# Performance work log

Measured on AMD Instinct MI355X. Metric: run time of the kernel, lower is better.

Reference implementation:

```python
import jax, jax.numpy as jnp
import numpy as np

E = 600000
N = 50000
H = 128
OE = 256


def swish(v):
    return v * jax.nn.sigmoid(v)


def setup_inputs() -> dict:
    key = jax.random.key(0)
    ks = jax.random.split(key, 16)
    inp = {
        "x": jax.random.normal(ks[0], (E, H), dtype=jnp.float32),
        "rbf": jax.random.normal(ks[1], (E, 6), dtype=jnp.float32),
        "i": jax.random.randint(ks[2], (E,), 0, N, dtype=jnp.int32),
        "edge_index": jax.random.randint(ks[3], (2, E), 0, N, dtype=jnp.int32),
        "edge_weight": jax.random.uniform(ks[4], (E,), dtype=jnp.float32),
        "batch": jax.random.randint(ks[5], (N,), 0, 32, dtype=jnp.int32),
        "num_nodes": N,
        "W_rbf": jax.random.normal(ks[6], (H, 6), dtype=jnp.float32) * 0.2,
        "W_up": jax.random.normal(ks[7], (OE, H), dtype=jnp.float32) * (1.0 / np.sqrt(H)),
        "b_up": jnp.zeros((OE,), dtype=jnp.float32),
        "W_l1": jax.random.normal(ks[8], (OE, OE), dtype=jnp.float32) * (1.0 / np.sqrt(OE)),
        "b_l1": jnp.zeros((OE,), dtype=jnp.float32),
        "W_l2": jax.random.normal(ks[9], (OE, OE), dtype=jnp.float32) * (1.0 / np.sqrt(OE)),
        "b_l2": jnp.zeros((OE,), dtype=jnp.float32),
        "W_l3": jax.random.normal(ks[10], (OE, OE), dtype=jnp.float32) * (1.0 / np.sqrt(OE)),
        "b_l3": jnp.zeros((OE,), dtype=jnp.float32),
        "W_out": jax.random.normal(ks[11], (1, OE), dtype=jnp.float32) * (1.0 / np.sqrt(OE)),
        "W_w": jax.random.normal(ks[12], (1, H), dtype=jnp.float32) * (1.0 / np.sqrt(H)),
        "b_w": jnp.zeros((1,), dtype=jnp.float32),
    }
    return inp


def reference(x, rbf, i, edge_index, edge_weight, batch, num_nodes,
              W_rbf, W_up, b_up, W_l1, b_l1, W_l2, b_l2, W_l3, b_l3,
              W_out, W_w, b_w):
    # edge_index / edge_weight are unused in the original forward.
    # x = lin_rbf(rbf) * x  -> [E, H]
    xe = (rbf @ W_rbf.T) * x
    # scatter-add edges -> nodes: [N, H]
    xn = jax.ops.segment_sum(xe, i, num_segments=num_nodes)
    # energy head: alpha = w_lin(x) before lin_up
    alpha = xn @ W_w.T + b_w  # [N, 1]
    x2 = xn @ W_up.T + b_up   # [N, OE]
    for W, b in ((W_l1, b_l1), (W_l2, b_l2), (W_l3, b_l3)):
        x2 = swish(x2 @ W.T + b)
    out = (x2 @ W_out.T) * alpha  # [N, 1]
    return (out, batch)
```

## Files before the change

### kernel.cpp

```cpp
#include <hip/hip_runtime.h>
#include <hip/hip_bf16.h>
#include <math.h>

#define E_CNT 600000
#define N_CNT 50000
#define H_DIM 128
#define OE_DIM 256

typedef __attribute__((ext_vector_type(8))) short short8;
typedef __attribute__((ext_vector_type(4))) float f32x4;

#define WS_OFF    0
#define WS_CNT    200016
#define WS_TEXC   400016
#define WS_BSUM   600720
#define WS_WUP    601744
#define WS_WL1    667280
#define WS_WL2    798352
#define WS_WL3    929424
#define WS_RANK   1060496
#define WS_XE     3460496

#define SCAN_NB 196
#define WCONV_NB 896

__global__ __launch_bounds__(256) void histwconv_kernel(
    const int* __restrict__ nid, int* __restrict__ counts,
    int* __restrict__ rank,
    const float* __restrict__ Wup, const float* __restrict__ Wl1,
    const float* __restrict__ Wl2, const float* __restrict__ Wl3,
    ushort* __restrict__ dUp, ushort* __restrict__ dL1,
    ushort* __restrict__ dL2, ushort* __restrict__ dL3)
{
    if (blockIdx.x < WCONV_NB) {
        int d = blockIdx.x * 256 + threadIdx.x;
        const float* W;
        ushort* dst;
        int K;
        if (d < 32768)       { W = Wup; dst = dUp; K = 128; }
        else if (d < 98304)  { d -= 32768;  W = Wl1; dst = dL1; K = 256; }
        else if (d < 163840) { d -= 98304;  W = Wl2; dst = dL2; K = 256; }
        else                 { d -= 163840; W = Wl3; dst = dL3; K = 256; }
        int j = d & 7;
        int l = (d >> 3) & 63;
        int KS = K >> 5;
        int ks = (d >> 9) % KS;
        int ot = (d >> 9) / KS;
        int k = ks * 32 + ((l >> 4) << 3) + j;
        int o = ot * 16 + (l & 15);
        __hip_bfloat16 h = __float2bfloat16(W[o * K + k]);
        dst[d] = *(const ushort*)&h;
    } else {
        int nb = gridDim.x - WCONV_NB;
        for (int e = (blockIdx.x - WCONV_NB) * 256 + threadIdx.x; e < E_CNT;
             e += nb * 256)
            rank[e] = atomicAdd(&counts[nid[e]], 1);
    }
}

__global__ __launch_bounds__(256) void scanA_kernel(const int* __restrict__ counts,
                                                    int* __restrict__ texc,
                                                    int* __restrict__ bsum)
{
    __shared__ int s[256];
    const int t = threadIdx.x;
    const int i = blockIdx.x * 256 + t;
    int v = (i < N_CNT) ? counts[i] : 0;
    s[t] = v;
    __syncthreads();
    for (int off = 1; off < 256; off <<= 1) {
        int u = (t >= off) ? s[t - off] : 0;
        __syncthreads();
        s[t] += u;
        __syncthreads();
    }
    texc[i] = s[t] - v;
    if (t == 255) bsum[blockIdx.x] = s[255];
}

__global__ __launch_bounds__(256) void scanC_kernel(const int* __restrict__ texc,
                                                    const int* __restrict__ bsum,
                                                    int* __restrict__ offs)
{
    __shared__ int red[256];
    const int t = threadIdx.x;
    int v = (t < (int)blockIdx.x && t < SCAN_NB) ? bsum[t] : 0;
    red[t] = v;
    __syncthreads();
    for (int off = 128; off >= 1; off >>= 1) {
        if (t < off) red[t] += red[t + off];
        __syncthreads();
    }
    const int boff = red[0];
    const int i = blockIdx.x * 256 + t;
    if (i < N_CNT) offs[i] = texc[i] + boff;
    if (i == 0) offs[N_CNT] = E_CNT;
}

__global__ __launch_bounds__(256, 4) void prepass_kernel(
    const float* __restrict__ x, const float* __restrict__ rbf,
    const int* __restrict__ nid, const int* __restrict__ rank,
    const int* __restrict__ offs, const float* __restrict__ W_rbf,
    ushort* __restrict__ xep)
{
    const int tid = threadIdx.x;
    const int lane = tid & 63;
    const int q = lane >> 4;
    const int p = lane & 15;
    const int h0 = p * 8;

    float wrb[8][6];
#pragma unroll
    for (int j = 0; j < 8; ++j)
#pragma unroll
        for (int k = 0; k < 6; ++k)
            wrb[j][k] = W_rbf[(h0 + j) * 6 + k];

    const int wid = (blockIdx.x * 256 + tid) >> 6;
    const int nw = (gridDim.x * 256) >> 6;
    const int nquad = E_CNT / 4;

    for (int t = wid; t < nquad; t += nw) {
        const int e = t * 4 + q;
        const int slot = offs[nid[e]] + rank[e];

        const float4 xa = *(const float4*)(x + (size_t)e * H_DIM + h0);
        const float4 xb = *(const float4*)(x + (size_t)e * H_DIM + h0 + 4);
        const float2* rp = (const float2*)(rbf + (size_t)e * 6);
        const float2 q0 = rp[0], q1 = rp[1], q2 = rp[2];
        const float r[6] = {q0.x, q0.y, q1.x, q1.y, q2.x, q2.y};

        float c[8];
#pragma unroll
        for (int j = 0; j < 8; ++j) {
            float cc = 0.f;
#pragma unroll
            for (int k = 0; k < 6; ++k) cc = fmaf(r[k], wrb[j][k], cc);
            c[j] = cc;
        }
        const float xv[8] = {xa.x, xa.y, xa.z, xa.w, xb.x, xb.y, xb.z, xb.w};
        ushort pk[8];
#pragma unroll
        for (int j = 0; j < 8; ++j) {
            __hip_bfloat16 h = __float2bfloat16(c[j] * xv[j]);
            pk[j] = *(const ushort*)&h;
        }
        *(int4*)(xep + (size_t)slot * H_DIM + h0) = *(const int4*)pk;
    }
}

#define MB 32
#define PITCH 264

template<int KS, bool SW>
__device__ __forceinline__ void layer(const ushort* __restrict__ Wsh,
                                      const float* __restrict__ bias,
                                      const ushort* in_s, ushort* out_s, int tid)
{
    const int w = tid >> 6, lane = tid & 63;
    const int l15 = lane & 15, lg = lane >> 4;

    f32x4 acc[2][2];
#pragma unroll
    for (int mi = 0; mi < 2; ++mi)
#pragma unroll
        for (int oi = 0; oi < 2; ++oi)
            acc[mi][oi] = (f32x4){0.f, 0.f, 0.f, 0.f};

#pragma unroll
    for (int ks = 0; ks < KS; ++ks) {
        short8 b0 = *(const short8*)(Wsh + (size_t)(((w * 2 + 0) * KS + ks) * 64 + lane) * 8);
        short8 b1 = *(const short8*)(Wsh + (size_t)(((w * 2 + 1) * KS + ks) * 64 + lane) * 8);
#pragma unroll
        for (int mi = 0; mi < 2; ++mi) {
            short8 a = *(const short8*)(in_s + (mi * 16 + l15) * PITCH + ks * 32 + lg * 8);
            acc[mi][0] = __builtin_amdgcn_mfma_f32_16x16x32_bf16(a, b0, acc[mi][0], 0, 0, 0);
            acc[mi][1] = __builtin_amdgcn_mfma_f32_16x16x32_bf16(a, b1, acc[mi][1], 0, 0, 0);
        }
    }

#pragma unroll
    for (int oi = 0; oi < 2; ++oi) {
        float bv = bias[(w * 2 + oi) * 16 + l15];
#pragma unroll
        for (int mi = 0; mi < 2; ++mi)
#pragma unroll
            for (int r = 0; r < 4; ++r) {
                float v = acc[mi][oi][r] + bv;
                if (SW) v = v / (1.f + __expf(-v));
                __hip_bfloat16 h = __float2bfloat16(v);
                out_s[(mi * 16 + lg * 4 + r) * PITCH + (w * 2 + oi) * 16 + l15] =
                    *(const ushort*)&h;
            }
    }
}

__global__ __launch_bounds__(512, 6) void fused_kernel(
    const ushort* __restrict__ xep,
    const int* __restrict__ offs,
    const float* __restrict__ W_w, const float* __restrict__ b_w,
    const ushort* __restrict__ Wup, const ushort* __restrict__ Wl1,
    const ushort* __restrict__ Wl2, const ushort* __restrict__ Wl3,
    const float* __restrict__ b_up, const float* __restrict__ b_l1,
    const float* __restrict__ b_l2, const float* __restrict__ b_l3,
    const float* __restrict__ W_out, const int* __restrict__ batch,
    float* __restrict__ out)
{
    __shared__ ushort sA[MB * PITCH];
    __shared__ ushort sB[MB * PITCH];
    __shared__ int s_off[MB + 1];
    __shared__ float s_alpha[MB];

    const int tid = threadIdx.x;
    const int w = tid >> 6, lane = tid & 63;
    const int node0 = blockIdx.x * MB;

    if (tid < MB) {
        int node = node0 + tid;
        if (node < N_CNT) out[N_CNT + node] = (float)batch[node];
    }
    if (tid < MB + 1)
        s_off[tid] = offs[min(node0 + tid, N_CNT)];
    __syncthreads();

    {
        const int eq = lane >> 4;
        const int p = lane & 15;
        float ww[8];
#pragma unroll
        for (int j = 0; j < 8; ++j) ww[j] = W_w[p * 8 + j];
        const float bw = b_w[0];

        for (int nl4 = 0; nl4 < 4; ++nl4) {
            const int nl = (w << 2) + nl4;
            const int ls = s_off[nl], le = s_off[nl + 1];
            float acc[8];
#pragma unroll
            for (int j = 0; j < 8; ++j) acc[j] = 0.f;

#pragma unroll 2
            for (int s = ls + eq; s < le; s += 4) {
                short8 rv = *(const short8*)(xep + (size_t)s * H_DIM + p * 8);
#pragma unroll
                for (int j = 0; j < 8; ++j) {
                    ushort u = (ushort)rv[j];
                    acc[j] += __bfloat162float(*(const __hip_bfloat16*)&u);
                }
            }
#pragma unroll
            for (int j = 0; j < 8; ++j) {
                acc[j] += __shfl_xor(acc[j], 16);
                acc[j] += __shfl_xor(acc[j], 32);
            }
            float part = 0.f;
#pragma unroll
            for (int j = 0; j < 8; ++j) part = fmaf(acc[j], ww[j], part);
            part += __shfl_xor(part, 1);
            part += __shfl_xor(part, 2);
            part += __shfl_xor(part, 4);
            part += __shfl_xor(part, 8);
            if (lane == 0) s_alpha[nl] = part + bw;
            if (eq == 0) {
                ushort pk[8];
#pragma unroll
                for (int j = 0; j < 8; ++j) {
                    __hip_bfloat16 h = __float2bfloat16(acc[j]);
                    pk[j] = *(const ushort*)&h;
                }
                *(int4*)(sA + nl * PITCH + p * 8) = *(const int4*)pk;
            }
        }
    }
    __syncthreads();

    layer<4, false>(Wup, b_up, sA, sB, tid);
    __syncthreads();
    layer<8, true>(Wl1, b_l1, sB, sA, tid);
    __syncthreads();
    layer<8, true>(Wl2, b_l2, sA, sB, tid);
    __syncthreads();
    layer<8, true>(Wl3, b_l3, sB, sA, tid);
    __syncthreads();

    {
        int nl = tid >> 4, q = tid & 15;
        const ushort* rowp = sA + nl * PITCH + q * 16;
        float sum = 0.f;
#pragma unroll
        for (int o = 0; o < 16; ++o) {
            __hip_bfloat16 h = *(const __hip_bfloat16*)(rowp + o);
            sum = fmaf(__bfloat162float(h), W_out[q * 16 + o], sum);
        }
        sum += __shfl_xor(sum, 1);
        sum += __shfl_xor(sum, 2);
        sum += __shfl_xor(sum, 4);
        sum += __shfl_xor(sum, 8);
        int node = node0 + nl;
        if (q == 0 && node < N_CNT) out[node] = sum * s_alpha[nl];
    }
}

extern "C" void kernel_launch(void* const* d_in, const int* in_sizes, int n_in,
                              void* d_out, int out_size, void* d_ws, size_t ws_size,
                              hipStream_t stream)
{
    const float* x      = (const float*)d_in[0];
    const float* rbf    = (const float*)d_in[1];
    const int*   nid    = (const int*)d_in[2];
    const int*   batch  = (const int*)d_in[5];
    const float* W_rbf  = (const float*)d_in[7];
    const float* W_up   = (const float*)d_in[8];
    const float* b_up   = (const float*)d_in[9];
    const float* W_l1   = (const float*)d_in[10];
    const float* b_l1   = (const float*)d_in[11];
    const float* W_l2   = (const float*)d_in[12];
    const float* b_l2   = (const float*)d_in[13];
    const float* W_l3   = (const float*)d_in[14];
    const float* b_l3   = (const float*)d_in[15];
    const float* W_out  = (const float*)d_in[16];
    const float* W_w    = (const float*)d_in[17];
    const float* b_w    = (const float*)d_in[18];

    char* ws = (char*)d_ws;
    int*    offs   = (int*)(ws + WS_OFF);
    int*    counts = (int*)(ws + WS_CNT);
    int*    texc   = (int*)(ws + WS_TEXC);
    int*    bsum   = (int*)(ws + WS_BSUM);
    ushort* WupS   = (ushort*)(ws + WS_WUP);
    ushort* Wl1S   = (ushort*)(ws + WS_WL1);
    ushort* Wl2S   = (ushort*)(ws + WS_WL2);
    ushort* Wl3S   = (ushort*)(ws + WS_WL3);
    int*    rank   = (int*)(ws + WS_RANK);
    ushort* xep    = (ushort*)(ws + WS_XE);
    float*  out    = (float*)d_out;

    hipMemsetAsync(counts, 0, N_CNT * sizeof(int), stream);
    histwconv_kernel<<<WCONV_NB + 1024, 256, 0, stream>>>(
        nid, counts, rank, W_up, W_l1, W_l2, W_l3, WupS, Wl1S, Wl2S, Wl3S);
    scanA_kernel<<<SCAN_NB, 256, 0, stream>>>(counts, texc, bsum);
    scanC_kernel<<<SCAN_NB, 256, 0, stream>>>(texc, bsum, offs);

    prepass_kernel<<<2048, 256, 0, stream>>>(x, rbf, nid, rank, offs, W_rbf, xep);

    fused_kernel<<<(N_CNT + MB - 1) / MB, 512, 0, stream>>>(
        xep, offs, W_w, b_w,
        WupS, Wl1S, Wl2S, Wl3S, b_up, b_l1, b_l2, b_l3, W_out, batch, out);
}
```

Measured before the change: 233.9 us.

## Write edge features in original order and gather via sorted edge-id list

The prepass now writes bf16 edge features contiguously in edge order instead of scattering each row to its sorted slot, and records a sorted-slot to edge-id map. The fused kernel stages chunks of edge ids in shared memory and gathers each edge row indirectly when reducing per node. This replaces scattered 256-byte writes with coalesced writes at the cost of scattered reads, an extra int array, chunked accumulation through bf16 shared memory (possible extra rounding), and lower occupancy bounds.

```diff
diff --git a/kernel.cpp b/kernel.cpp
--- a/kernel.cpp
+++ b/kernel.cpp
@@ -19,7 +19,8 @@
 #define WS_WL2    798352
 #define WS_WL3    929424
 #define WS_RANK   1060496
-#define WS_XE     3460496
+#define WS_EIDS   3460496
+#define WS_XE     5860496
 
 #define SCAN_NB 196
 #define WCONV_NB 896
@@ -101,7 +102,7 @@
     const float* __restrict__ x, const float* __restrict__ rbf,
     const int* __restrict__ nid, const int* __restrict__ rank,
     const int* __restrict__ offs, const float* __restrict__ W_rbf,
-    ushort* __restrict__ xep)
+    ushort* __restrict__ xe16, int* __restrict__ eids)
 {
     const int tid = threadIdx.x;
     const int lane = tid & 63;
@@ -122,7 +123,9 @@
 
     for (int t = wid; t < nquad; t += nw) {
         const int e = t * 4 + q;
-        const int slot = offs[nid[e]] + rank[e];
+
+        if (p == 0)
+            eids[offs[nid[e]] + rank[e]] = e;
 
         const float4 xa = *(const float4*)(x + (size_t)e * H_DIM + h0);
         const float4 xb = *(const float4*)(x + (size_t)e * H_DIM + h0 + 4);
@@ -145,12 +148,13 @@
             __hip_bfloat16 h = __float2bfloat16(c[j] * xv[j]);
             pk[j] = *(const ushort*)&h;
         }
-        *(int4*)(xep + (size_t)slot * H_DIM + h0) = *(const int4*)pk;
+        *(int4*)(xe16 + (size_t)e * H_DIM + h0) = *(const int4*)pk;
     }
 }
 
 #define MB 32
 #define PITCH 264
+#define EMAX 640
 
 template<int KS, bool SW>
 __device__ __forceinline__ void layer(const ushort* __restrict__ Wsh,
@@ -195,9 +199,9 @@
     }
 }
 
-__global__ __launch_bounds__(512, 6) void fused_kernel(
-    const ushort* __restrict__ xep,
-    const int* __restrict__ offs,
+__global__ __launch_bounds__(512, 4) void fused_kernel(
+    const ushort* __restrict__ xe16,
+    const int* __restrict__ offs, const int* __restrict__ eids,
     const float* __restrict__ W_w, const float* __restrict__ b_w,
     const ushort* __restrict__ Wup, const ushort* __restrict__ Wl1,
     const ushort* __restrict__ Wl2, const ushort* __restrict__ Wl3,
@@ -208,6 +212,7 @@
 {
     __shared__ ushort sA[MB * PITCH];
     __shared__ ushort sB[MB * PITCH];
+    __shared__ int s_eids[EMAX];
     __shared__ int s_off[MB + 1];
     __shared__ float s_alpha[MB];
 
@@ -222,6 +227,10 @@
     if (tid < MB + 1)
         s_off[tid] = offs[min(node0 + tid, N_CNT)];
     __syncthreads();
+
+    const int s0 = s_off[0];
+    const int tot = s_off[MB] - s0;
+    const int nchunks = (tot + EMAX - 1) / EMAX;
 
     {
         const int eq = lane >> 4;
@@ -231,43 +240,67 @@
         for (int j = 0; j < 8; ++j) ww[j] = W_w[p * 8 + j];
         const float bw = b_w[0];
 
-        for (int nl4 = 0; nl4 < 4; ++nl4) {
-            const int nl = (w << 2) + nl4;
-            const int ls = s_off[nl], le = s_off[nl + 1];
-            float acc[8];
-#pragma unroll
-            for (int j = 0; j < 8; ++j) acc[j] = 0.f;
-
-#pragma unroll 2
-            for (int s = ls + eq; s < le; s += 4) {
-                short8 rv = *(const short8*)(xep + (size_t)s * H_DIM + p * 8);
+        for (int c = 0; c < nchunks; ++c) {
+            const int cs = c * EMAX;
+            const int ce = min(cs + EMAX, tot);
+            __syncthreads();
+            for (int t = tid + cs; t < ce; t += 512) s_eids[t - cs] = eids[s0 + t];
+            __syncthreads();
+
+            for (int nl4 = 0; nl4 < 4; ++nl4) {
+                const int nl = (w << 2) + nl4;
+                const int ls = max(s_off[nl] - s0, cs);
+                const int le = min(s_off[nl + 1] - s0, ce);
+                float acc[8];
+#pragma unroll
+                for (int j = 0; j < 8; ++j) acc[j] = 0.f;
+
+                for (int s = ls + eq; s < le; s += 4) {
+                    const int e = s_eids[s - cs];
+                    short8 rv = *(const short8*)(xe16 + (size_t)e * H_DIM + p * 8);
+#pragma unroll
+                    for (int j = 0; j < 8; ++j) {
+                        ushort u = (ushort)rv[j];
+                        acc[j] += __bfloat162float(*(const __hip_bfloat16*)&u);
+                    }
+                }
 #pragma unroll
                 for (int j = 0; j < 8; ++j) {
-                    ushort u = (ushort)rv[j];
-                    acc[j] += __bfloat162float(*(const __hip_bfloat16*)&u);
+                    acc[j] += __shfl_xor(acc[j], 16);
+                    acc[j] += __shfl_xor(acc[j], 32);
                 }
-            }
-#pragma unroll
-            for (int j = 0; j < 8; ++j) {
-                acc[j] += __shfl_xor(acc[j], 16);
-                acc[j] += __shfl_xor(acc[j], 32);
-            }
-            float part = 0.f;
-#pragma unroll
-            for (int j = 0; j < 8; ++j) part = fmaf(acc[j], ww[j], part);
-            part += __shfl_xor(part, 1);
-            part += __shfl_xor(part, 2);
-            part += __shfl_xor(part, 4);
-            part += __shfl_xor(part, 8);
-            if (lane == 0) s_alpha[nl] = part + bw;
-            if (eq == 0) {
-                ushort pk[8];
-#pragma unroll
-                for (int j = 0; j < 8; ++j) {
-                    __hip_bfloat16 h = __float2bfloat16(acc[j]);
-                    pk[j] = *(const ushort*)&h;
+                float part = 0.f;
+#pragma unroll
+                for (int j = 0; j < 8; ++j) part = fmaf(acc[j], ww[j], part);
+                part += __shfl_xor(part, 1);
+                part += __shfl_xor(part, 2);
+                part += __shfl_xor(part, 4);
+                part += __shfl_xor(part, 8);
+                if (lane == 0) {
+                    if (c > 0) s_alpha[nl] += part;
+                    else       s_alpha[nl] = part + bw;
                 }
-                *(int4*)(sA + nl * PITCH + p * 8) = *(const int4*)pk;
+                if (eq == 0) {
+                    ushort4* dp0 = (ushort4*)(sA + nl * PITCH + p * 8);
+                    if (c > 0) {
+                        ushort4 o0 = dp0[0], o1 = dp0[1];
+                        acc[0] += __bfloat162float(*(const __hip_bfloat16*)&o0.x);
+                        acc[1] += __bfloat162float(*(const __hip_bfloat16*)&o0.y);
+                        acc[2] += __bfloat162float(*(const __hip_bfloat16*)&o0.z);
+                        acc[3] += __bfloat162float(*(const __hip_bfloat16*)&o0.w);
+                        acc[4] += __bfloat162float(*(const __hip_bfloat16*)&o1.x);
+                        acc[5] += __bfloat162float(*(const __hip_bfloat16*)&o1.y);
+                        acc[6] += __bfloat162float(*(const __hip_bfloat16*)&o1.z);
+                        acc[7] += __bfloat162float(*(const __hip_bfloat16*)&o1.w);
+                    }
+                    ushort pk[8];
+#pragma unroll
+                    for (int j = 0; j < 8; ++j) {
+                        __hip_bfloat16 h = __float2bfloat16(acc[j]);
+                        pk[j] = *(const ushort*)&h;
+                    }
+                    *(int4*)(sA + nl * PITCH + p * 8) = *(const int4*)pk;
+                }
             }
         }
     }
@@ -331,7 +364,8 @@
     ushort* Wl2S   = (ushort*)(ws + WS_WL2);
     ushort* Wl3S   = (ushort*)(ws + WS_WL3);
     int*    rank   = (int*)(ws + WS_RANK);
-    ushort* xep    = (ushort*)(ws + WS_XE);
+    int*    eids   = (int*)(ws + WS_EIDS);
+    ushort* xe16   = (ushort*)(ws + WS_XE);
     float*  out    = (float*)d_out;
 
     hipMemsetAsync(counts, 0, N_CNT * sizeof(int), stream);
@@ -340,9 +374,10 @@
     scanA_kernel<<<SCAN_NB, 256, 0, stream>>>(counts, texc, bsum);
     scanC_kernel<<<SCAN_NB, 256, 0, stream>>>(texc, bsum, offs);
 
-    prepass_kernel<<<2048, 256, 0, stream>>>(x, rbf, nid, rank, offs, W_rbf, xep);
+    prepass_kernel<<<2048, 256, 0, stream>>>(x, rbf, nid, rank, offs, W_rbf,
+                                             xe16, eids);
 
     fused_kernel<<<(N_CNT + MB - 1) / MB, 512, 0, stream>>>(
-        xep, offs, W_w, b_w,
+        xe16, offs, eids, W_w, b_w,
         WupS, Wl1S, Wl2S, Wl3S, b_up, b_l1, b_l2, b_l3, W_out, batch, out);
 }
```

After: 244.8 us. 4.7% more time.
